# Optimization experiments

Hardware: AMD Instinct MI355X
Metric: run time of the kernel (lower is better)

## Reference

```python
import jax, jax.numpy as jnp
import numpy as np

LOSS_WEIGHT = 0.01  # balancing_loss_alpha


def setup_inputs() -> dict:
    key = jax.random.key(0)
    L, T, E = 32, 16384, 64  # num_layers, tokens, n_routed_experts
    router_logits = jax.random.normal(key, (L, T, E), dtype=jnp.float32)
    return {
        "router_logits": router_logits,
        "n_routed_experts": E,
        "num_experts_per_tok": 8,
    }


def reference(router_logits, n_routed_experts, num_experts_per_tok):
    # loss_type == 'softmax', global_average single-device path
    L, T, E = router_logits.shape
    logits = router_logits.astype(jnp.float32)
    routing_weights = jax.nn.softmax(logits, axis=-1)  # [L, T, E]
    # top-k expert selection per token
    _, selected = jax.lax.top_k(routing_weights, num_experts_per_tok)  # [L, T, K]
    # per-layer histogram of expert assignments (== offset + histc in torch)
    counts = jax.vmap(lambda s: jnp.bincount(s.reshape(-1), length=n_routed_experts))(
        selected
    )  # [L, E] int
    tokens_per_expert = counts.astype(routing_weights.dtype)
    scale = n_routed_experts / (T * num_experts_per_tok)
    rw_mean = routing_weights.mean(axis=1)  # [L, E]
    loss = (scale * (tokens_per_expert * rw_mean).sum(-1)).sum()
    return loss * LOSS_WEIGHT
```

## Files before the change

kernel.cpp:

```cpp
#include <hip/hip_runtime.h>
#include <float.h>

#define NL 32
#define NT 16384
#define NE 64
#define NK 8
#define LOG2E 1.4426950408889634f

#define DPP_QUAD_XOR1 0xB1
#define DPP_QUAD_XOR2 0x4E
#define DPP_ROW_ROR4  0x124
#define DPP_ROW_ROR8  0x128

template <int CTRL>
__device__ __forceinline__ float dppmv(float v) {
    return __int_as_float(
        __builtin_amdgcn_update_dpp(0, __float_as_int(v), CTRL, 0xF, 0xF, true));
}

__device__ __forceinline__ float grp_max(float v) {
    v = fmaxf(v, dppmv<DPP_QUAD_XOR1>(v));
    v = fmaxf(v, dppmv<DPP_QUAD_XOR2>(v));
    v = fmaxf(v, dppmv<DPP_ROW_ROR4>(v));
    v = fmaxf(v, dppmv<DPP_ROW_ROR8>(v));
    return v;
}
__device__ __forceinline__ float grp_sum(float v) {
    v = v + dppmv<DPP_QUAD_XOR1>(v);
    v = v + dppmv<DPP_QUAD_XOR2>(v);
    v = v + dppmv<DPP_ROW_ROR4>(v);
    v = v + dppmv<DPP_ROW_ROR8>(v);
    return v;
}

__device__ __forceinline__ void ce(float& a, float& b) {
    float hi = fmaxf(a, b);
    float lo = fminf(a, b);
    a = hi; b = lo;
}

__global__ __launch_bounds__(256, 8) void bl_main(const float* __restrict__ logits,
                                                  float* __restrict__ g_w,
                                                  float* __restrict__ g_c) {
    const int tid  = threadIdx.x;
    const int lane = tid & 63;
    const int wv   = tid >> 6;
    const long slab = ((long)blockIdx.x * 4 + wv) * 64;
    const int layer = (int)(slab >> 14);

    const float4* p = (const float4*)(logits + slab * NE);

    float wacc[4] = {0.f, 0.f, 0.f, 0.f};
    float cacc[4] = {0.f, 0.f, 0.f, 0.f};

    float4 buf[2];
    buf[0] = p[0 * 64 + lane];
    buf[1] = p[1 * 64 + lane];

#pragma unroll
    for (int j = 0; j < 16; ++j) {
        const float4 cur = buf[j & 1];
        if (j + 2 < 16) buf[j & 1] = p[(j + 2) * 64 + lane];

        const float x0 = __builtin_amdgcn_exp2f(cur.x * LOG2E);
        const float x1 = __builtin_amdgcn_exp2f(cur.y * LOG2E);
        const float x2 = __builtin_amdgcn_exp2f(cur.z * LOG2E);
        const float x3 = __builtin_amdgcn_exp2f(cur.w * LOG2E);

        const float den = grp_sum((x0 + x1) + (x2 + x3));
        const float inv = __builtin_amdgcn_rcpf(den);

        float q0 = x0, q1 = x1, q2 = x2, q3 = x3;
        ce(q0, q1); ce(q2, q3); ce(q0, q2); ce(q1, q3); ce(q1, q2);

        float thr = 0.f;
#pragma unroll
        for (int k = 0; k < NK; ++k) {
            const float m = grp_max(q0);
            thr = m;
            if (k < NK - 1) {
                const bool hit = (q0 == m);
                q0 = hit ? q1 : q0;
                q1 = hit ? q2 : q1;
                q2 = hit ? q3 : q2;
                q3 = hit ? -1.0f : q3;
            }
        }

        cacc[0] += (x0 >= thr) ? 1.f : 0.f;
        cacc[1] += (x1 >= thr) ? 1.f : 0.f;
        cacc[2] += (x2 >= thr) ? 1.f : 0.f;
        cacc[3] += (x3 >= thr) ? 1.f : 0.f;

        wacc[0] = fmaf(x0, inv, wacc[0]);
        wacc[1] = fmaf(x1, inv, wacc[1]);
        wacc[2] = fmaf(x2, inv, wacc[2]);
        wacc[3] = fmaf(x3, inv, wacc[3]);
    }

#pragma unroll
    for (int r = 0; r < 4; ++r) {
        wacc[r] += __shfl_xor(wacc[r], 16);
        wacc[r] += __shfl_xor(wacc[r], 32);
        cacc[r] += __shfl_xor(cacc[r], 16);
        cacc[r] += __shfl_xor(cacc[r], 32);
    }

    __shared__ float comb[2][NE][4];
    if (lane < 16) {
#pragma unroll
        for (int r = 0; r < 4; ++r) {
            comb[0][lane * 4 + r][wv] = wacc[r];
            comb[1][lane * 4 + r][wv] = cacc[r];
        }
    }
    __syncthreads();
    if (tid < 128) {
        const int s = tid >> 6, e = tid & 63;
        const float val = comb[s][e][0] + comb[s][e][1] + comb[s][e][2] + comb[s][e][3];
        float* dst = s ? g_c : g_w;
        atomicAdd(&dst[layer * NE + e], val);
    }
}

__global__ void bl_final(const float* __restrict__ g_w,
                         const float* __restrict__ g_c,
                         float* __restrict__ out) {
    __shared__ float red[256];
    float p = 0.f;
    for (int i = threadIdx.x; i < NL * NE; i += 256) p += g_c[i] * g_w[i];
    red[threadIdx.x] = p;
    __syncthreads();
    for (int s = 128; s > 0; s >>= 1) {
        if (threadIdx.x < s) red[threadIdx.x] += red[threadIdx.x + s];
        __syncthreads();
    }
    if (threadIdx.x == 0) {
        const float factor = (float)(0.01 * ((double)NE / ((double)NT * NK)) / (double)NT);
        out[0] = red[0] * factor;
    }
}

extern "C" void kernel_launch(void* const* d_in, const int* in_sizes, int n_in,
                              void* d_out, int out_size, void* d_ws, size_t ws_size,
                              hipStream_t stream) {
    const float* logits = (const float*)d_in[0];
    float* g_w = (float*)d_ws;
    float* g_c = g_w + NL * NE;

    hipMemsetAsync(d_ws, 0, 2 * NL * NE * sizeof(float), stream);
    bl_main<<<dim3(2048), dim3(256), 0, stream>>>(logits, g_w, g_c);
    bl_final<<<dim3(1), dim3(256), 0, stream>>>(g_w, g_c, (float*)d_out);
}
```

Measured before the change: 52.76 us.

## Stage logits via global_load_lds and replace atomics with per-block partials

Loads of logits now go straight into LDS through global_load_lds, using a 4-deep per-wave ring buffer with explicit vmcnt waits, instead of register double-buffering. Per-layer atomicAdds and the memset are replaced by per-block partial writes, which a 1024-thread final kernel reduces. This removes the memset launch and atomic contention. In exchange it adds LDS traffic and a larger serial reduction in the final kernel, which reads 2048x128 partials.

```diff
diff --git a/kernel.cpp b/kernel.cpp
--- a/kernel.cpp
+++ b/kernel.cpp
@@ -5,6 +5,7 @@
 #define NT 16384
 #define NE 64
 #define NK 8
+#define BPL 64
 #define LOG2E 1.4426950408889634f
 
 #define DPP_QUAD_XOR1 0xB1
@@ -39,28 +40,42 @@
     a = hi; b = lo;
 }
 
+__device__ __forceinline__ void load_lds16(const float4* gsrc, float4* lds_dst) {
+    __builtin_amdgcn_global_load_lds(
+        (__attribute__((address_space(1))) void*)gsrc,
+        (__attribute__((address_space(3))) void*)lds_dst, 16, 0, 0);
+}
+
 __global__ __launch_bounds__(256, 8) void bl_main(const float* __restrict__ logits,
-                                                  float* __restrict__ g_w,
-                                                  float* __restrict__ g_c) {
+                                                  float* __restrict__ partials) {
     const int tid  = threadIdx.x;
     const int lane = tid & 63;
     const int wv   = tid >> 6;
     const long slab = ((long)blockIdx.x * 4 + wv) * 64;
-    const int layer = (int)(slab >> 14);
 
     const float4* p = (const float4*)(logits + slab * NE);
+
+    __shared__ float4 stage[4][4][64];
+    __shared__ float comb[2][NE][4];
 
     float wacc[4] = {0.f, 0.f, 0.f, 0.f};
     float cacc[4] = {0.f, 0.f, 0.f, 0.f};
 
-    float4 buf[2];
-    buf[0] = p[0 * 64 + lane];
-    buf[1] = p[1 * 64 + lane];
+    load_lds16(p + 0 * 64 + lane, &stage[wv][0][0]);
+    load_lds16(p + 1 * 64 + lane, &stage[wv][1][0]);
 
 #pragma unroll
     for (int j = 0; j < 16; ++j) {
-        const float4 cur = buf[j & 1];
-        if (j + 2 < 16) buf[j & 1] = p[(j + 2) * 64 + lane];
+        if (j < 14) {
+            load_lds16(p + (j + 2) * 64 + lane, &stage[wv][(j + 2) & 3][0]);
+            asm volatile("s_waitcnt vmcnt(2)" ::: "memory");
+        } else if (j == 14) {
+            asm volatile("s_waitcnt vmcnt(1)" ::: "memory");
+        } else {
+            asm volatile("s_waitcnt vmcnt(0)" ::: "memory");
+        }
+
+        const float4 cur = stage[wv][j & 3][lane];
 
         const float x0 = __builtin_amdgcn_exp2f(cur.x * LOG2E);
         const float x1 = __builtin_amdgcn_exp2f(cur.y * LOG2E);
@@ -106,7 +121,6 @@
         cacc[r] += __shfl_xor(cacc[r], 32);
     }
 
-    __shared__ float comb[2][NE][4];
     if (lane < 16) {
 #pragma unroll
         for (int r = 0; r < 4; ++r) {
@@ -118,24 +132,35 @@
     if (tid < 128) {
         const int s = tid >> 6, e = tid & 63;
         const float val = comb[s][e][0] + comb[s][e][1] + comb[s][e][2] + comb[s][e][3];
-        float* dst = s ? g_c : g_w;
-        atomicAdd(&dst[layer * NE + e], val);
+        partials[(long)blockIdx.x * 128 + s * 64 + e] = val;
     }
 }
 
-__global__ void bl_final(const float* __restrict__ g_w,
-                         const float* __restrict__ g_c,
-                         float* __restrict__ out) {
-    __shared__ float red[256];
-    float p = 0.f;
-    for (int i = threadIdx.x; i < NL * NE; i += 256) p += g_c[i] * g_w[i];
-    red[threadIdx.x] = p;
+__global__ __launch_bounds__(1024) void bl_final(const float* __restrict__ partials,
+                                                 float* __restrict__ out) {
+    const int tid  = threadIdx.x;
+    const int e    = tid & 63;
+    const int lsub = tid >> 6;
+    float acc = 0.f;
+#pragma unroll
+    for (int half = 0; half < 2; ++half) {
+        const int l = lsub + 16 * half;
+        float wsum = 0.f, csum = 0.f;
+        for (int b = 0; b < BPL; ++b) {
+            const float* base = partials + ((long)(l * BPL + b) * 128);
+            wsum += base[e];
+            csum += base[64 + e];
+        }
+        acc += wsum * csum;
+    }
+    __shared__ float red[1024];
+    red[tid] = acc;
     __syncthreads();
-    for (int s = 128; s > 0; s >>= 1) {
-        if (threadIdx.x < s) red[threadIdx.x] += red[threadIdx.x + s];
+    for (int s = 512; s > 0; s >>= 1) {
+        if (tid < s) red[tid] += red[tid + s];
         __syncthreads();
     }
-    if (threadIdx.x == 0) {
+    if (tid == 0) {
         const float factor = (float)(0.01 * ((double)NE / ((double)NT * NK)) / (double)NT);
         out[0] = red[0] * factor;
     }
@@ -145,10 +170,8 @@
                               void* d_out, int out_size, void* d_ws, size_t ws_size,
                               hipStream_t stream) {
     const float* logits = (const float*)d_in[0];
-    float* g_w = (float*)d_ws;
-    float* g_c = g_w + NL * NE;
+    float* partials = (float*)d_ws;
 
-    hipMemsetAsync(d_ws, 0, 2 * NL * NE * sizeof(float), stream);
-    bl_main<<<dim3(2048), dim3(256), 0, stream>>>(logits, g_w, g_c);
-    bl_final<<<dim3(1), dim3(256), 0, stream>>>(g_w, g_c, (float*)d_out);
+    bl_main<<<dim3(2048), dim3(256), 0, stream>>>(logits, partials);
+    bl_final<<<dim3(1), dim3(1024), 0, stream>>>(partials, (float*)d_out);
 }
```

New measurement: 56.26 us. 1.07x slower.

## Fuse final reduction into main kernel via last-block counter, deepen prefetch

Applied to the files above, without the earlier changes.

The separate single-block final kernel is removed. Each block now increments a global counter after its atomics, and the last block to finish computes the dot product and writes the loss. Loads now use nontemporal hints, and the register prefetch ring grows from 2 to 6 float4 buffers to keep more memory requests in flight. This saves one kernel launch and its gap, at the cost of an extra fence and atomic per block and some register pressure.

```diff
diff --git a/kernel.cpp b/kernel.cpp
--- a/kernel.cpp
+++ b/kernel.cpp
@@ -5,7 +5,10 @@
 #define NT 16384
 #define NE 64
 #define NK 8
+#define NBLK 2048
 #define LOG2E 1.4426950408889634f
+
+typedef float floatx4 __attribute__((ext_vector_type(4)));
 
 #define DPP_QUAD_XOR1 0xB1
 #define DPP_QUAD_XOR2 0x4E
@@ -39,28 +42,30 @@
     a = hi; b = lo;
 }
 
-__global__ __launch_bounds__(256, 8) void bl_main(const float* __restrict__ logits,
-                                                  float* __restrict__ g_w,
-                                                  float* __restrict__ g_c) {
+__global__ __launch_bounds__(256, 8) void bl_fused(const float* __restrict__ logits,
+                                                   float* __restrict__ g_w,
+                                                   float* __restrict__ g_c,
+                                                   unsigned int* __restrict__ cnt,
+                                                   float* __restrict__ out) {
     const int tid  = threadIdx.x;
     const int lane = tid & 63;
     const int wv   = tid >> 6;
     const long slab = ((long)blockIdx.x * 4 + wv) * 64;
     const int layer = (int)(slab >> 14);
 
-    const float4* p = (const float4*)(logits + slab * NE);
+    const floatx4* p = (const floatx4*)(logits + slab * NE);
 
     float wacc[4] = {0.f, 0.f, 0.f, 0.f};
     float cacc[4] = {0.f, 0.f, 0.f, 0.f};
 
-    float4 buf[2];
-    buf[0] = p[0 * 64 + lane];
-    buf[1] = p[1 * 64 + lane];
+    floatx4 buf[6];
+#pragma unroll
+    for (int j = 0; j < 6; ++j) buf[j] = __builtin_nontemporal_load(&p[j * 64 + lane]);
 
 #pragma unroll
     for (int j = 0; j < 16; ++j) {
-        const float4 cur = buf[j & 1];
-        if (j + 2 < 16) buf[j & 1] = p[(j + 2) * 64 + lane];
+        const floatx4 cur = buf[j % 6];
+        if (j + 6 < 16) buf[j % 6] = __builtin_nontemporal_load(&p[(j + 6) * 64 + lane]);
 
         const float x0 = __builtin_amdgcn_exp2f(cur.x * LOG2E);
         const float x1 = __builtin_amdgcn_exp2f(cur.y * LOG2E);
@@ -107,6 +112,7 @@
     }
 
     __shared__ float comb[2][NE][4];
+    __shared__ int last_flag;
     if (lane < 16) {
 #pragma unroll
         for (int r = 0; r < 4; ++r) {
@@ -121,23 +127,38 @@
         float* dst = s ? g_c : g_w;
         atomicAdd(&dst[layer * NE + e], val);
     }
-}
+    __syncthreads();
 
-__global__ void bl_final(const float* __restrict__ g_w,
-                         const float* __restrict__ g_c,
-                         float* __restrict__ out) {
-    __shared__ float red[256];
-    float p = 0.f;
-    for (int i = threadIdx.x; i < NL * NE; i += 256) p += g_c[i] * g_w[i];
-    red[threadIdx.x] = p;
+    if (tid == 0) {
+        __threadfence();
+        const unsigned int old =
+            __hip_atomic_fetch_add(cnt, 1u, __ATOMIC_ACQ_REL, __HIP_MEMORY_SCOPE_AGENT);
+        last_flag = (old == NBLK - 1) ? 1 : 0;
+    }
     __syncthreads();
-    for (int s = 128; s > 0; s >>= 1) {
-        if (threadIdx.x < s) red[threadIdx.x] += red[threadIdx.x + s];
+
+    if (last_flag) {
+        float acc = 0.f;
+#pragma unroll
+        for (int k = 0; k < 8; ++k) {
+            const int i = tid + k * 256;
+            const float w = __hip_atomic_load(&g_w[i], __ATOMIC_RELAXED,
+                                              __HIP_MEMORY_SCOPE_AGENT);
+            const float c = __hip_atomic_load(&g_c[i], __ATOMIC_RELAXED,
+                                              __HIP_MEMORY_SCOPE_AGENT);
+            acc = fmaf(w, c, acc);
+        }
+        __shared__ float red[256];
+        red[tid] = acc;
         __syncthreads();
-    }
-    if (threadIdx.x == 0) {
-        const float factor = (float)(0.01 * ((double)NE / ((double)NT * NK)) / (double)NT);
-        out[0] = red[0] * factor;
+        for (int s = 128; s > 0; s >>= 1) {
+            if (tid < s) red[tid] += red[tid + s];
+            __syncthreads();
+        }
+        if (tid == 0) {
+            const float factor = (float)(0.01 * ((double)NE / ((double)NT * NK)) / (double)NT);
+            out[0] = red[0] * factor;
+        }
     }
 }
 
@@ -147,8 +168,8 @@
     const float* logits = (const float*)d_in[0];
     float* g_w = (float*)d_ws;
     float* g_c = g_w + NL * NE;
+    unsigned int* cnt = (unsigned int*)(g_c + NL * NE);
 
-    hipMemsetAsync(d_ws, 0, 2 * NL * NE * sizeof(float), stream);
-    bl_main<<<dim3(2048), dim3(256), 0, stream>>>(logits, g_w, g_c);
-    bl_final<<<dim3(1), dim3(256), 0, stream>>>(g_w, g_c, (float*)d_out);
+    (void)hipMemsetAsync(d_ws, 0, 2 * NL * NE * sizeof(float) + sizeof(unsigned int), stream);
+    bl_fused<<<dim3(NBLK), dim3(256), 0, stream>>>(logits, g_w, g_c, cnt, (float*)d_out);
 }
```

Result: slower. 183.0 us (+246.8%).
